# Optimization experiments

Hardware: AMD Instinct MI355X
Metric: run time of the kernel (lower is better)

The kernel has to match this reference:

```python
import jax, jax.numpy as jnp
import numpy as np

V, E, D_ENC, H, A, NF, K = 96, 64, 256, 256, 128, 10, 5
B, T_ENC, T_TGT = 64, 1024, 256


def setup_inputs() -> dict:
    key = jax.random.key(0)
    ks = jax.random.split(key, 16)
    s = 0.05
    emb = jax.random.normal(ks[0], (V, E), jnp.float32) * s
    emb = emb.at[0].set(0.0)  # padding_idx=0
    inp = {
        "encoder_outputs": jax.random.normal(ks[1], (B, T_ENC, D_ENC), jnp.float32),
        "encoder_lengths": jax.random.randint(ks[2], (B,), 1, T_ENC + 1),
        "targets": jax.random.randint(ks[3], (B, T_TGT), 0, V),
        "emb": emb,
        "W_ih": jax.random.normal(ks[4], (4 * H, E + D_ENC), jnp.float32) * s,
        "W_hh": jax.random.normal(ks[5], (4 * H, H), jnp.float32) * s,
        "b_ih": jax.random.normal(ks[6], (4 * H,), jnp.float32) * s,
        "b_hh": jax.random.normal(ks[7], (4 * H,), jnp.float32) * s,
        "conv_w": jax.random.normal(ks[8], (NF, 1, K), jnp.float32) * s,
        "W_enc": jax.random.normal(ks[9], (A, D_ENC), jnp.float32) * s,
        "W_dec": jax.random.normal(ks[10], (A, H), jnp.float32) * s,
        "W_loc": jax.random.normal(ks[11], (A, NF), jnp.float32) * s,
        "v_w": jax.random.normal(ks[12], (1, A), jnp.float32) * s,
        "out_w1": jax.random.normal(ks[13], (H, H + D_ENC), jnp.float32) * s,
        "out_b1": jax.random.normal(ks[14], (H,), jnp.float32) * s,
        "out_w2": jax.random.normal(ks[15], (V, H), jnp.float32) * s,
        "out_b2": jnp.zeros((V,), jnp.float32),
    }
    return inp


def _forward(encoder_outputs, encoder_lengths, targets, emb, W_ih, W_hh, b_ih,
             b_hh, conv_w, W_enc, W_dec, W_loc, v_w, out_w1, out_b1, out_w2, out_b2):
    dtype = encoder_outputs.dtype
    b, t_enc, d_enc = encoder_outputs.shape
    mask = jnp.arange(t_enc)[None, :] < encoder_lengths[:, None]  # [B, T_enc]
    enc_proj = encoder_outputs @ W_enc.T  # [B, T_enc, A] (weights fixed -> hoisted)
    bias = b_ih + b_hh
    pad = (K - 1) // 2

    tok_emb = emb[targets[:, :-1]]          # [B, T_dec, E]
    tok_emb = jnp.swapaxes(tok_emb, 0, 1)   # [T_dec, B, E] for scan

    h0 = jnp.zeros((b, H), dtype)
    c0 = jnp.zeros((b, H), dtype)
    ctx0 = jnp.zeros((b, d_enc), dtype)
    aw0 = jnp.full((b, t_enc), 1.0 / t_enc, dtype)

    def step(carry, e_t):
        h, c, ctx, aw = carry
        # LSTM cell (PyTorch gate order i, f, g, o)
        x = jnp.concatenate([e_t, ctx], axis=-1)            # [B, E+D_enc]
        gates = x @ W_ih.T + h @ W_hh.T + bias              # [B, 4H]
        i, f, g, o = jnp.split(gates, 4, axis=-1)
        c = jax.nn.sigmoid(f) * c + jax.nn.sigmoid(i) * jnp.tanh(g)
        h = jax.nn.sigmoid(o) * jnp.tanh(c)
        # location-sensitive attention
        loc = jax.lax.conv_general_dilated(aw[:, None, :], conv_w, (1,),
                                           [(pad, pad)],
                                           dimension_numbers=("NCH", "OIH", "NCH"))
        loc = jnp.swapaxes(loc, 1, 2)                       # [B, T_enc, NF]
        energy_in = enc_proj + (h @ W_dec.T)[:, None, :] + loc @ W_loc.T
        energy = jnp.tanh(energy_in) @ v_w[0]               # [B, T_enc]
        energy = jnp.where(mask, energy, -1e9)
        aw = jax.nn.softmax(energy, axis=1)
        ctx = jnp.einsum("bt,btd->bd", aw, encoder_outputs)
        # output MLP (dropout = identity at eval)
        hid = jnp.tanh(jnp.concatenate([h, ctx], axis=-1) @ out_w1.T + out_b1)
        logits = hid @ out_w2.T + out_b2                    # [B, V]
        return (h, c, ctx, aw), logits

    _, logits = jax.lax.scan(step, (h0, c0, ctx0, aw0), tok_emb)
    return jnp.swapaxes(logits, 0, 1)  # [B, T_dec, V]


def reference(encoder_outputs, encoder_lengths, targets, emb, W_ih, W_hh, b_ih,
              b_hh, conv_w, W_enc, W_dec, W_loc, v_w, out_w1, out_b1, out_w2, out_b2):
    return _forward(encoder_outputs, encoder_lengths, targets, emb, W_ih, W_hh,
                    b_ih, b_hh, conv_w, W_enc, W_dec, W_loc, v_w, out_w1,
                    out_b1, out_w2, out_b2)
```

## Files before the change

### kernel.cpp

```cpp
#include <hip/hip_runtime.h>
#include <hip/hip_bf16.h>

#define BB   64
#define TENC 1024
#define DENC 256
#define HN   256
#define AN   128
#define NFC  10
#define EMBD 64
#define VN   96
#define TT   255

typedef unsigned short u16;

__device__ __forceinline__ float fsig(float x){ return 1.0f/(1.0f+__expf(-x)); }
__device__ __forceinline__ float ftanh(float x){ return 1.0f - 2.0f/(1.0f+__expf(2.0f*x)); }
__device__ __forceinline__ float b2f(u16 v){ return __uint_as_float(((unsigned)v) << 16); }
__device__ __forceinline__ u16 f2b(float x){
    __hip_bfloat16 h = __float2bfloat16(x);
    return *reinterpret_cast<u16*>(&h);
}
__device__ __forceinline__ float4 ld_bf4(const u16* p){
    ushort4 v = *(const ushort4*)p;
    return make_float4(b2f(v.x), b2f(v.y), b2f(v.z), b2f(v.w));
}

struct Params {
    const u16* encb; const u16* enc_projb; const u16* WdecTb;
    const float* conv_w; const float* W_loc; const float* v_w;
    const int* lengths; const int* targets; const float* emb;
    const float* WcombP; const float* biasw;
    const float* W1T; const float* out_b1; const float* W2T; const float* out_b2;
    float* e0; float* e1; float* ctxU0; float* ctxU1; float* SU0; float* SU1;
    float* h0; float* h1; float* c_st; float* hidA; float* hidB;
    float* out;
};

__global__ void k_prep(const float* __restrict__ enc,
                       const float* __restrict__ W_ih, const float* __restrict__ W_hh,
                       const float* __restrict__ b_ih, const float* __restrict__ b_hh,
                       const float* __restrict__ W_dec, const float* __restrict__ out_w1,
                       const float* __restrict__ out_w2,
                       u16* __restrict__ encb, u16* __restrict__ WdecTb,
                       float* __restrict__ WcombP, float* __restrict__ biasw,
                       float* __restrict__ W1T, float* __restrict__ W2T,
                       float* __restrict__ e_init, float* __restrict__ S_init)
{
    int tid = blockIdx.x*blockDim.x + threadIdx.x;
    int tot = blockDim.x*gridDim.x;
    for (size_t i = tid; i < (size_t)BB*TENC*DENC; i += tot) encb[i] = f2b(enc[i]);
    for (int i = tid; i < 576*1024; i += tot){
        int k = i >> 10, rp = i & 1023;
        int ug = rp >> 4, q = rp & 15, gidx = q >> 2, ul = q & 3;
        int g = gidx*256 + ug*4 + ul;
        WcombP[i] = (k < 320) ? W_ih[(size_t)g*320 + k] : W_hh[(size_t)g*256 + (k-320)];
    }
    for (int i = tid; i < 1024; i += tot) biasw[i] = b_ih[i] + b_hh[i];
    for (int i = tid; i < 256*128; i += tot){ int u = i>>7, a = i&127; WdecTb[i] = f2b(W_dec[a*256 + u]); }
    for (int i = tid; i < 512*256; i += tot){ int k = i>>8, r = i&255; W1T[i] = out_w1[(size_t)r*512 + k]; }
    for (int i = tid; i < 256*96;  i += tot){ int k = i/96, v = i - k*96; W2T[i] = out_w2[(size_t)v*256 + k]; }
    for (int i = tid; i < BB*TENC; i += tot) e_init[i] = 1.0f;
    for (int i = tid; i < BB; i += tot) S_init[i] = (float)TENC;
}

__global__ __launch_bounds__(128) void k_encproj(const float* __restrict__ enc,
                                                 const float* __restrict__ W_enc,
                                                 u16* __restrict__ enc_projb)
{
    __shared__ float rows[32][256];
    int r0 = blockIdx.x * 32;
    for (int i = threadIdx.x; i < 32*256; i += 128)
        rows[i>>8][i&255] = enc[(size_t)r0*256 + i];
    __syncthreads();
    int a = threadIdx.x;
    float acc[32];
    #pragma unroll
    for (int r=0;r<32;r++) acc[r]=0.f;
    const float* w = W_enc + a*256;
    for (int d=0; d<256; d+=4){
        float4 wv = *(const float4*)(w + d);
        #pragma unroll
        for (int r=0;r<32;r++){
            float4 rv = *(const float4*)(&rows[r][d]);
            acc[r] += wv.x*rv.x + wv.y*rv.y + wv.z*rv.z + wv.w*rv.w;
        }
    }
    for (int r=0;r<32;r++) enc_projb[(size_t)(r0+r)*AN + a] = f2b(acc[r]);
}

union alignas(16) SMemCell {
    struct { float xh[8][584]; float part[4][16][9]; float gates[8][17]; } gat;
};
union alignas(16) SMemAtt {
    struct { float hdec[128]; float part[256]; float ehalo[68]; float cw[52];
             float loc[64][11]; float wlocT[10*128]; float evals[64];
             float ep[64][33]; float wacc[4][256]; } att;
    struct { float xh[8][520]; float part[4][16][9]; } hidm;
    struct { float hs[8][260]; float part[4][32][9]; } lgt;
};

__global__ __launch_bounds__(256) void k_cell(Params P, int t)
{
    __shared__ SMemCell u;
    const int blk = blockIdx.x, tid = threadIdx.x;
    const int wr = t & 1;
    const float* ctxU_r = wr ? P.ctxU0 : P.ctxU1;
    float*       ctxU_w = wr ? P.ctxU1 : P.ctxU0;
    const float* SU_r   = wr ? P.SU0   : P.SU1;
    float*       SU_w   = wr ? P.SU1   : P.SU0;
    const float* h_old  = wr ? P.h0    : P.h1;
    float*       h_new  = wr ? P.h1    : P.h0;

    const int ug = blk & 63, bg = blk >> 6;
    const int b0 = bg*8;
    if (ug == 1){
        for (int i = tid; i < 8*DENC; i += 256) ctxU_w[b0*DENC + i] = 0.f;
        if (tid < 8) SU_w[b0 + tid] = 0.f;
    }
    for (int i = tid; i < 8*EMBD; i += 256){
        int bl = i>>6, j = i&63;
        int tok = P.targets[(b0+bl)*256 + t];
        u.gat.xh[bl][j] = P.emb[tok*EMBD + j];
    }
    for (int i = tid; i < 8*HN; i += 256){
        int bl = i>>8, d = i&255;
        u.gat.xh[bl][320+d] = (t == 0) ? 0.f : h_old[(b0+bl)*HN + d];
    }
    for (int i = tid; i < 8*DENC; i += 256){
        int bl = i>>8, d = i&255;
        u.gat.xh[bl][64+d] = (t == 0) ? 0.f
            : ctxU_r[(b0+bl)*DENC + d] * (1.0f/SU_r[b0+bl]);
    }
    __syncthreads();
    {
        const int kq = tid >> 6, lane = tid & 63, rl = lane & 15, blq = lane >> 4;
        const int rowP = ug*16 + rl, bl0 = blq*2;
        const float* wp  = P.WcombP + (size_t)(kq*144)*1024 + rowP;
        const float* x0p = &u.gat.xh[bl0][kq*144];
        const float* x1p = &u.gat.xh[bl0+1][kq*144];
        float s0 = 0.f, s1 = 0.f;
        for (int k = 0; k < 144; k += 4){
            float w0 = wp[0], w1 = wp[1024], w2 = wp[2048], w3 = wp[3072]; wp += 4096;
            float4 xa = *(const float4*)(x0p + k);
            float4 xb = *(const float4*)(x1p + k);
            s0 += w0*xa.x + w1*xa.y + w2*xa.z + w3*xa.w;
            s1 += w0*xb.x + w1*xb.y + w2*xb.z + w3*xb.w;
        }
        u.gat.part[kq][rl][bl0] = s0; u.gat.part[kq][rl][bl0+1] = s1;
    }
    __syncthreads();
    if (tid < 128){
        int bl = tid >> 4, rl = tid & 15;
        float s = u.gat.part[0][rl][bl] + u.gat.part[1][rl][bl]
                + u.gat.part[2][rl][bl] + u.gat.part[3][rl][bl];
        int gidx = rl >> 2, ul = rl & 3;
        u.gat.gates[bl][rl] = s + P.biasw[gidx*256 + ug*4 + ul];
    }
    __syncthreads();
    if (tid < 32){
        int bl = tid >> 2, ul = tid & 3;
        int bgl = b0 + bl, unit = ug*4 + ul;
        float gi = u.gat.gates[bl][0+ul],  gf = u.gat.gates[bl][4+ul];
        float gg = u.gat.gates[bl][8+ul],  go = u.gat.gates[bl][12+ul];
        float cold = (t == 0) ? 0.f : P.c_st[bgl*HN + unit];
        float cn = fsig(gf)*cold + fsig(gi)*ftanh(gg);
        P.c_st[bgl*HN + unit] = cn;
        h_new[bgl*HN + unit] = fsig(go)*ftanh(cn);
    }
}

__global__ __launch_bounds__(256) void k_att(Params P, int t)
{
    __shared__ SMemAtt u;
    const int blk = blockIdx.x, tid = threadIdx.x;
    const int wr = t & 1;
    const float* ctxU_r = wr ? P.ctxU0 : P.ctxU1;
    float*       ctxU_w = wr ? P.ctxU1 : P.ctxU0;
    const float* SU_r   = wr ? P.SU0   : P.SU1;
    float*       SU_w   = wr ? P.SU1   : P.SU0;
    const float* h_old  = wr ? P.h0    : P.h1;
    const float* h_new  = wr ? P.h1    : P.h0;
    const float* hid_pv = wr ? P.hidA  : P.hidB;
    float*       hid_nw = wr ? P.hidB  : P.hidA;
    const float* e_prev = wr ? P.e0    : P.e1;
    float*       e_new  = wr ? P.e1    : P.e0;

    if (blk < 512){
        if (t > 254) return;
        const int b = blk >> 3;
        const int q = blk & 7;
        const int len = P.lengths[b];
        const float invS = 1.0f / SU_r[b];

        if (tid < 50) u.att.cw[tid] = P.conv_w[tid];
        for (int i = tid; i < 1280; i += 256){
            int f = i >> 7, a = i & 127;
            u.att.wlocT[f*128 + a] = P.W_loc[a*NFC + f];
        }
        {
            int a = tid & 127, half = tid >> 7;
            const u16* wd = P.WdecTb + (size_t)(half*128)*AN + a;
            const float* hb = h_new + b*HN + half*128;
            float s0 = 0.f, s1 = 0.f;
            #pragma unroll 4
            for (int uu = 0; uu < 128; uu += 2){
                s0 += hb[uu]   * b2f(wd[(size_t)uu*AN]);
                s1 += hb[uu+1] * b2f(wd[(size_t)(uu+1)*AN]);
            }
            u.att.part[tid] = s0 + s1;
        }
        __syncthreads();
        if (tid < 128) u.att.hdec[tid] = u.att.part[tid] + u.att.part[tid+128];
        __syncthreads();

        for (int kk = 0; kk < 2; kk++){
            const int ch = q + 8*kk;
            const int t0 = ch*64;
            float* e_row = e_new + b*TENC + t0;
            int nv = len - t0; nv = nv < 0 ? 0 : (nv > 64 ? 64 : nv);
            if (nv == 0){
                if (tid < 64) e_row[tid] = 0.f;
                continue;
            }
            __syncthreads();
            if (tid < 68){
                int g = t0 - 2 + tid;
                u.att.ehalo[tid] = (g >= 0 && g < TENC) ? e_prev[b*TENC + g] : 0.f;
            }
            __syncthreads();
            if (tid < 64){
                #pragma unroll
                for (int f = 0; f < NFC; f++){
                    float s = 0.f;
                    #pragma unroll
                    for (int k2 = 0; k2 < 5; k2++) s += u.att.ehalo[tid+k2] * u.att.cw[f*5+k2];
                    u.att.loc[tid][f] = s * invS;
                }
            }
            __syncthreads();

            {
                const int ag = tid & 31, pg = tid >> 5;
                const int a0 = ag*4;
                float4 hd4 = *(const float4*)&u.att.hdec[a0];
                float4 vv  = *(const float4*)(P.v_w + a0);
                const u16* epr = P.enc_projb + ((size_t)(b*TENC + t0))*AN + a0;
                #pragma unroll
                for (int i = 0; i < 8; i++){
                    int p = pg*8 + i;
                    if (p < nv){
                        float4 er = ld_bf4(epr + (size_t)p*AN);
                        float x0 = er.x + hd4.x, x1 = er.y + hd4.y;
                        float x2 = er.z + hd4.z, x3 = er.w + hd4.w;
                        #pragma unroll
                        for (int f = 0; f < NFC; f++){
                            float lf = u.att.loc[p][f];
                            const float* wla = &u.att.wlocT[f*128 + a0];
                            x0 += lf*wla[0]; x1 += lf*wla[1]; x2 += lf*wla[2]; x3 += lf*wla[3];
                        }
                        u.att.ep[p][ag] = vv.x*ftanh(x0) + vv.y*ftanh(x1)
                                        + vv.z*ftanh(x2) + vv.w*ftanh(x3);
                    }
                }
            }
            __syncthreads();

            if (tid < 64){
                int p = tid;
                float e = 0.f;
                if (p < nv){
                    float s0 = 0.f, s1 = 0.f;
                    #pragma unroll
                    for (int j = 0; j < 32; j += 2){ s0 += u.att.ep[p][j]; s1 += u.att.ep[p][j+1]; }
                    e = __expf(s0 + s1);
                }
                u.att.evals[p] = e;
                e_row[p] = e;
                float se = e;
                #pragma unroll
                for (int off = 32; off; off >>= 1) se += __shfl_xor(se, off);
                if (tid == 0) atomicAdd(SU_w + b, se);
            }
            __syncthreads();

            {
                const int dq = tid & 63, pq = tid >> 6;
                const u16* encb = P.encb + ((size_t)(b*TENC + t0))*DENC + dq*4;
                float ax=0.f, ay=0.f, az=0.f, aw=0.f;
                for (int i = 0; i < 16; i++){
                    int p = pq + i*4;
                    if (p < nv){
                        float ev = u.att.evals[p];
                        float4 ex = ld_bf4(encb + (size_t)p*DENC);
                        ax += ev*ex.x; ay += ev*ex.y; az += ev*ex.z; aw += ev*ex.w;
                    }
                }
                float4 r; r.x=ax; r.y=ay; r.z=az; r.w=aw;
                *(float4*)&u.att.wacc[pq][dq*4] = r;
            }
            __syncthreads();
            {
                int d = tid;
                float s = u.att.wacc[0][d] + u.att.wacc[1][d]
                        + u.att.wacc[2][d] + u.att.wacc[3][d];
                atomicAdd(ctxU_w + b*DENC + d, s);
            }
            __syncthreads();
        }
        return;
    }

    if (blk < 640){
        if (!(t >= 1 && t <= 255)) return;
        int hb = blk - 512;
        int bg = hb >> 4, rg = hb & 15;
        int b0 = bg*8, r0 = rg*16;
        for (int i = tid; i < 8*HN; i += 256){
            int bl = i>>8, d = i&255;
            u.hidm.xh[bl][d] = h_old[(b0+bl)*HN + d];
        }
        for (int i = tid; i < 8*DENC; i += 256){
            int bl = i>>8, d = i&255;
            u.hidm.xh[bl][256+d] = ctxU_r[(b0+bl)*DENC + d] * (1.0f/SU_r[b0+bl]);
        }
        __syncthreads();
        {
            const int kq = tid >> 6, lane = tid & 63, rl = lane & 15, blq = lane >> 4;
            const int bl0 = blq*2;
            const float* wp  = P.W1T + (size_t)(kq*128)*256 + (r0 + rl);
            const float* x0p = &u.hidm.xh[bl0][kq*128];
            const float* x1p = &u.hidm.xh[bl0+1][kq*128];
            float s0 = 0.f, s1 = 0.f;
            for (int k = 0; k < 128; k += 4){
                float w0 = wp[0], w1 = wp[256], w2 = wp[512], w3 = wp[768]; wp += 1024;
                float4 xa = *(const float4*)(x0p + k);
                float4 xb = *(const float4*)(x1p + k);
                s0 += w0*xa.x + w1*xa.y + w2*xa.z + w3*xa.w;
                s1 += w0*xb.x + w1*xb.y + w2*xb.z + w3*xb.w;
            }
            u.hidm.part[kq][rl][bl0] = s0; u.hidm.part[kq][rl][bl0+1] = s1;
        }
        __syncthreads();
        if (tid < 128){
            int bl = tid >> 4, rl = tid & 15;
            int r = r0 + rl;
            float s = u.hidm.part[0][rl][bl] + u.hidm.part[1][rl][bl]
                    + u.hidm.part[2][rl][bl] + u.hidm.part[3][rl][bl];
            hid_nw[(b0+bl)*HN + r] = ftanh(s + P.out_b1[r]);
        }
        return;
    }

    {
        if (t < 2) return;
        int lt = blk - 640;
        int bgr = lt/3, vg = lt%3;
        int b0 = bgr*8, v0 = vg*32;
        for (int i = tid; i < 8*HN; i += 256){
            int bl = i>>8, d = i&255;
            u.lgt.hs[bl][d] = hid_pv[(b0+bl)*HN + d];
        }
        __syncthreads();
        {
            const int kq = tid >> 6, lane = tid & 63, vl = lane & 31, blq = lane >> 5;
            const int bl0 = blq*4;
            const float* wp = P.W2T + (size_t)(kq*64)*96 + (v0 + vl);
            float a4[4] = {0.f,0.f,0.f,0.f};
            for (int k = 0; k < 64; k += 4){
                float w0 = wp[0], w1 = wp[96], w2 = wp[192], w3 = wp[288]; wp += 384;
                #pragma unroll
                for (int j = 0; j < 4; j++){
                    float4 x = *(const float4*)&u.lgt.hs[bl0+j][kq*64 + k];
                    a4[j] += w0*x.x + w1*x.y + w2*x.z + w3*x.w;
                }
            }
            #pragma unroll
            for (int j = 0; j < 4; j++) u.lgt.part[kq][vl][bl0+j] = a4[j];
        }
        __syncthreads();
        {
            int bl = tid >> 5, vl = tid & 31;
            int v = v0 + vl;
            float s = u.lgt.part[0][vl][bl] + u.lgt.part[1][vl][bl]
                    + u.lgt.part[2][vl][bl] + u.lgt.part[3][vl][bl];
            P.out[((size_t)(b0+bl)*TT + (t-2))*VN + v] = s + P.out_b2[v];
        }
    }
}

extern "C" void kernel_launch(void* const* d_in, const int* in_sizes, int n_in,
                              void* d_out, int out_size, void* d_ws, size_t ws_size,
                              hipStream_t stream)
{
    const float* enc     = (const float*)d_in[0];
    const int*   lengths = (const int*)  d_in[1];
    const int*   targets = (const int*)  d_in[2];
    const float* emb     = (const float*)d_in[3];
    const float* W_ih    = (const float*)d_in[4];
    const float* W_hh    = (const float*)d_in[5];
    const float* b_ih    = (const float*)d_in[6];
    const float* b_hh    = (const float*)d_in[7];
    const float* conv_w  = (const float*)d_in[8];
    const float* W_enc   = (const float*)d_in[9];
    const float* W_dec   = (const float*)d_in[10];
    const float* W_loc   = (const float*)d_in[11];
    const float* v_w     = (const float*)d_in[12];
    const float* out_w1  = (const float*)d_in[13];
    const float* out_b1  = (const float*)d_in[14];
    const float* out_w2  = (const float*)d_in[15];
    const float* out_b2  = (const float*)d_in[16];
    float* out = (float*)d_out;

    float* ws = (float*)d_ws;
    size_t off = 0;
    auto alloc = [&](size_t n){ float* p = ws + off; off += n; return p; };
    u16*   encb      = (u16*)  alloc((size_t)BB*TENC*DENC/2);
    u16*   enc_projb = (u16*)  alloc((size_t)BB*TENC*AN/2);
    u16*   WdecTb    = (u16*)  alloc(256*128/2);
    float* WcombP    = alloc(576*1024);
    float* biasw     = alloc(1024);
    float* W1T       = alloc(512*256);
    float* W2T       = alloc(256*96);
    float* e0        = alloc(BB*TENC);
    float* e1        = alloc(BB*TENC);
    float* ctxU0     = alloc(BB*DENC);
    float* ctxU1     = alloc(BB*DENC);
    float* SU0       = alloc(BB);
    float* SU1       = alloc(BB);
    float* h0        = alloc(BB*HN);
    float* h1        = alloc(BB*HN);
    float* c_st      = alloc(BB*HN);
    float* hidA      = alloc(BB*HN);
    float* hidB      = alloc(BB*HN);
    if (off * sizeof(float) > ws_size) return;

    k_prep<<<dim3(512), dim3(256), 0, stream>>>(enc, W_ih, W_hh, b_ih, b_hh, W_dec,
                                                out_w1, out_w2,
                                                encb, WdecTb, WcombP, biasw, W1T, W2T,
                                                e1, SU1);
    k_encproj<<<dim3(2048), dim3(128), 0, stream>>>(enc, W_enc, enc_projb);

    Params pr;
    pr.encb = encb; pr.enc_projb = enc_projb; pr.WdecTb = WdecTb;
    pr.conv_w = conv_w; pr.W_loc = W_loc; pr.v_w = v_w;
    pr.lengths = lengths; pr.targets = targets; pr.emb = emb;
    pr.WcombP = WcombP; pr.biasw = biasw;
    pr.W1T = W1T; pr.out_b1 = out_b1; pr.W2T = W2T; pr.out_b2 = out_b2;
    pr.e0 = e0; pr.e1 = e1; pr.ctxU0 = ctxU0; pr.ctxU1 = ctxU1;
    pr.SU0 = SU0; pr.SU1 = SU1; pr.h0 = h0; pr.h1 = h1;
    pr.c_st = c_st; pr.hidA = hidA; pr.hidB = hidB; pr.out = out;

    for (int t = 0; t <= 256; t++){
        if (t <= 254)
            k_cell<<<dim3(512), dim3(256), 0, stream>>>(pr, t);
        k_att<<<dim3(664), dim3(256), 0, stream>>>(pr, t);
    }
}
```

Before: 12.09 ms.

## Rebalance per-step kernels: move conv and output MLP into cell kernel, split attention finer

Each timestep is reorganised. The cell kernel now also runs, in 64 extra blocks, the location convolution (written to a bf16 buffer), the output hidden layer and the logits, one batch row per block. The attention kernel becomes 1024 blocks, one per (batch, 64-position chunk), with W_loc held in registers and the convolution results read from global memory. The goal is to spread attention work across more blocks, remove the per-chunk conv sync chain and shorten the critical path. In exchange it adds a global round-trip for the conv features and rounds them to bf16, and the per-row MLP blocks do scalar matvecs with less weight reuse.

After: 12.37 ms. 2.3% more time.

```diff
diff --git a/kernel.cpp b/kernel.cpp
--- a/kernel.cpp
+++ b/kernel.cpp
@@ -33,21 +33,21 @@
     const float* W1T; const float* out_b1; const float* W2T; const float* out_b2;
     float* e0; float* e1; float* ctxU0; float* ctxU1; float* SU0; float* SU1;
     float* h0; float* h1; float* c_st; float* hidA; float* hidB;
+    u16* locb;
     float* out;
 };
 
-__global__ void k_prep(const float* __restrict__ enc,
+__global__ void k_prep(Params P, const float* __restrict__ enc,
                        const float* __restrict__ W_ih, const float* __restrict__ W_hh,
                        const float* __restrict__ b_ih, const float* __restrict__ b_hh,
                        const float* __restrict__ W_dec, const float* __restrict__ out_w1,
-                       const float* __restrict__ out_w2,
-                       u16* __restrict__ encb, u16* __restrict__ WdecTb,
-                       float* __restrict__ WcombP, float* __restrict__ biasw,
-                       float* __restrict__ W1T, float* __restrict__ W2T,
-                       float* __restrict__ e_init, float* __restrict__ S_init)
+                       const float* __restrict__ out_w2)
 {
     int tid = blockIdx.x*blockDim.x + threadIdx.x;
     int tot = blockDim.x*gridDim.x;
+    u16* encb = (u16*)P.encb;  u16* WdecTb = (u16*)P.WdecTb;
+    float* WcombP = (float*)P.WcombP; float* biasw = (float*)P.biasw;
+    float* W1T = (float*)P.W1T; float* W2T = (float*)P.W2T;
     for (size_t i = tid; i < (size_t)BB*TENC*DENC; i += tot) encb[i] = f2b(enc[i]);
     for (int i = tid; i < 576*1024; i += tot){
         int k = i >> 10, rp = i & 1023;
@@ -59,8 +59,8 @@
     for (int i = tid; i < 256*128; i += tot){ int u = i>>7, a = i&127; WdecTb[i] = f2b(W_dec[a*256 + u]); }
     for (int i = tid; i < 512*256; i += tot){ int k = i>>8, r = i&255; W1T[i] = out_w1[(size_t)r*512 + k]; }
     for (int i = tid; i < 256*96;  i += tot){ int k = i/96, v = i - k*96; W2T[i] = out_w2[(size_t)v*256 + k]; }
-    for (int i = tid; i < BB*TENC; i += tot) e_init[i] = 1.0f;
-    for (int i = tid; i < BB; i += tot) S_init[i] = (float)TENC;
+    for (int i = tid; i < BB*TENC; i += tot) P.e1[i] = 1.0f;
+    for (int i = tid; i < BB; i += tot) P.SU1[i] = (float)TENC;
 }
 
 __global__ __launch_bounds__(128) void k_encproj(const float* __restrict__ enc,
@@ -88,20 +88,18 @@
     for (int r=0;r<32;r++) enc_projb[(size_t)(r0+r)*AN + a] = f2b(acc[r]);
 }
 
-union alignas(16) SMemCell {
+union alignas(16) SMemU {
     struct { float xh[8][584]; float part[4][16][9]; float gates[8][17]; } gat;
-};
-union alignas(16) SMemAtt {
-    struct { float hdec[128]; float part[256]; float ehalo[68]; float cw[52];
-             float loc[64][11]; float wlocT[10*128]; float evals[64];
+    struct { float hbuf[256]; float part[256]; float loc[64][11]; float evals[64];
              float ep[64][33]; float wacc[4][256]; } att;
-    struct { float xh[8][520]; float part[4][16][9]; } hidm;
-    struct { float hs[8][260]; float part[4][32][9]; } lgt;
+    struct { float erow[1036]; float cw[52]; } convt;
+    struct { float xh[512]; } hid2;
+    struct { float hs[256]; } lg2;
 };
 
 __global__ __launch_bounds__(256) void k_cell(Params P, int t)
 {
-    __shared__ SMemCell u;
+    __shared__ SMemU u;
     const int blk = blockIdx.x, tid = threadIdx.x;
     const int wr = t & 1;
     const float* ctxU_r = wr ? P.ctxU0 : P.ctxU1;
@@ -110,281 +108,239 @@
     float*       SU_w   = wr ? P.SU1   : P.SU0;
     const float* h_old  = wr ? P.h0    : P.h1;
     float*       h_new  = wr ? P.h1    : P.h0;
-
-    const int ug = blk & 63, bg = blk >> 6;
-    const int b0 = bg*8;
-    if (ug == 1){
-        for (int i = tid; i < 8*DENC; i += 256) ctxU_w[b0*DENC + i] = 0.f;
-        if (tid < 8) SU_w[b0 + tid] = 0.f;
-    }
-    for (int i = tid; i < 8*EMBD; i += 256){
-        int bl = i>>6, j = i&63;
-        int tok = P.targets[(b0+bl)*256 + t];
-        u.gat.xh[bl][j] = P.emb[tok*EMBD + j];
-    }
-    for (int i = tid; i < 8*HN; i += 256){
-        int bl = i>>8, d = i&255;
-        u.gat.xh[bl][320+d] = (t == 0) ? 0.f : h_old[(b0+bl)*HN + d];
-    }
-    for (int i = tid; i < 8*DENC; i += 256){
-        int bl = i>>8, d = i&255;
-        u.gat.xh[bl][64+d] = (t == 0) ? 0.f
-            : ctxU_r[(b0+bl)*DENC + d] * (1.0f/SU_r[b0+bl]);
-    }
-    __syncthreads();
-    {
-        const int kq = tid >> 6, lane = tid & 63, rl = lane & 15, blq = lane >> 4;
-        const int rowP = ug*16 + rl, bl0 = blq*2;
-        const float* wp  = P.WcombP + (size_t)(kq*144)*1024 + rowP;
-        const float* x0p = &u.gat.xh[bl0][kq*144];
-        const float* x1p = &u.gat.xh[bl0+1][kq*144];
-        float s0 = 0.f, s1 = 0.f;
-        for (int k = 0; k < 144; k += 4){
-            float w0 = wp[0], w1 = wp[1024], w2 = wp[2048], w3 = wp[3072]; wp += 4096;
-            float4 xa = *(const float4*)(x0p + k);
-            float4 xb = *(const float4*)(x1p + k);
-            s0 += w0*xa.x + w1*xa.y + w2*xa.z + w3*xa.w;
-            s1 += w0*xb.x + w1*xb.y + w2*xb.z + w3*xb.w;
-        }
-        u.gat.part[kq][rl][bl0] = s0; u.gat.part[kq][rl][bl0+1] = s1;
-    }
-    __syncthreads();
-    if (tid < 128){
-        int bl = tid >> 4, rl = tid & 15;
-        float s = u.gat.part[0][rl][bl] + u.gat.part[1][rl][bl]
-                + u.gat.part[2][rl][bl] + u.gat.part[3][rl][bl];
-        int gidx = rl >> 2, ul = rl & 3;
-        u.gat.gates[bl][rl] = s + P.biasw[gidx*256 + ug*4 + ul];
-    }
-    __syncthreads();
-    if (tid < 32){
-        int bl = tid >> 2, ul = tid & 3;
-        int bgl = b0 + bl, unit = ug*4 + ul;
-        float gi = u.gat.gates[bl][0+ul],  gf = u.gat.gates[bl][4+ul];
-        float gg = u.gat.gates[bl][8+ul],  go = u.gat.gates[bl][12+ul];
-        float cold = (t == 0) ? 0.f : P.c_st[bgl*HN + unit];
-        float cn = fsig(gf)*cold + fsig(gi)*ftanh(gg);
-        P.c_st[bgl*HN + unit] = cn;
-        h_new[bgl*HN + unit] = fsig(go)*ftanh(cn);
-    }
-}
-
-__global__ __launch_bounds__(256) void k_att(Params P, int t)
-{
-    __shared__ SMemAtt u;
-    const int blk = blockIdx.x, tid = threadIdx.x;
-    const int wr = t & 1;
-    const float* ctxU_r = wr ? P.ctxU0 : P.ctxU1;
-    float*       ctxU_w = wr ? P.ctxU1 : P.ctxU0;
-    const float* SU_r   = wr ? P.SU0   : P.SU1;
-    float*       SU_w   = wr ? P.SU1   : P.SU0;
-    const float* h_old  = wr ? P.h0    : P.h1;
-    const float* h_new  = wr ? P.h1    : P.h0;
     const float* hid_pv = wr ? P.hidA  : P.hidB;
     float*       hid_nw = wr ? P.hidB  : P.hidA;
     const float* e_prev = wr ? P.e0    : P.e1;
-    float*       e_new  = wr ? P.e1    : P.e0;
 
     if (blk < 512){
         if (t > 254) return;
-        const int b = blk >> 3;
-        const int q = blk & 7;
-        const int len = P.lengths[b];
-        const float invS = 1.0f / SU_r[b];
-
-        if (tid < 50) u.att.cw[tid] = P.conv_w[tid];
-        for (int i = tid; i < 1280; i += 256){
-            int f = i >> 7, a = i & 127;
-            u.att.wlocT[f*128 + a] = P.W_loc[a*NFC + f];
-        }
-        {
-            int a = tid & 127, half = tid >> 7;
-            const u16* wd = P.WdecTb + (size_t)(half*128)*AN + a;
-            const float* hb = h_new + b*HN + half*128;
-            float s0 = 0.f, s1 = 0.f;
-            #pragma unroll 4
-            for (int uu = 0; uu < 128; uu += 2){
-                s0 += hb[uu]   * b2f(wd[(size_t)uu*AN]);
-                s1 += hb[uu+1] * b2f(wd[(size_t)(uu+1)*AN]);
-            }
-            u.att.part[tid] = s0 + s1;
-        }
-        __syncthreads();
-        if (tid < 128) u.att.hdec[tid] = u.att.part[tid] + u.att.part[tid+128];
-        __syncthreads();
-
-        for (int kk = 0; kk < 2; kk++){
-            const int ch = q + 8*kk;
-            const int t0 = ch*64;
-            float* e_row = e_new + b*TENC + t0;
-            int nv = len - t0; nv = nv < 0 ? 0 : (nv > 64 ? 64 : nv);
-            if (nv == 0){
-                if (tid < 64) e_row[tid] = 0.f;
-                continue;
-            }
-            __syncthreads();
-            if (tid < 68){
-                int g = t0 - 2 + tid;
-                u.att.ehalo[tid] = (g >= 0 && g < TENC) ? e_prev[b*TENC + g] : 0.f;
-            }
-            __syncthreads();
-            if (tid < 64){
-                #pragma unroll
-                for (int f = 0; f < NFC; f++){
-                    float s = 0.f;
-                    #pragma unroll
-                    for (int k2 = 0; k2 < 5; k2++) s += u.att.ehalo[tid+k2] * u.att.cw[f*5+k2];
-                    u.att.loc[tid][f] = s * invS;
-                }
-            }
-            __syncthreads();
-
-            {
-                const int ag = tid & 31, pg = tid >> 5;
-                const int a0 = ag*4;
-                float4 hd4 = *(const float4*)&u.att.hdec[a0];
-                float4 vv  = *(const float4*)(P.v_w + a0);
-                const u16* epr = P.enc_projb + ((size_t)(b*TENC + t0))*AN + a0;
-                #pragma unroll
-                for (int i = 0; i < 8; i++){
-                    int p = pg*8 + i;
-                    if (p < nv){
-                        float4 er = ld_bf4(epr + (size_t)p*AN);
-                        float x0 = er.x + hd4.x, x1 = er.y + hd4.y;
-                        float x2 = er.z + hd4.z, x3 = er.w + hd4.w;
-                        #pragma unroll
-                        for (int f = 0; f < NFC; f++){
-                            float lf = u.att.loc[p][f];
-                            const float* wla = &u.att.wlocT[f*128 + a0];
-                            x0 += lf*wla[0]; x1 += lf*wla[1]; x2 += lf*wla[2]; x3 += lf*wla[3];
-                        }
-                        u.att.ep[p][ag] = vv.x*ftanh(x0) + vv.y*ftanh(x1)
-                                        + vv.z*ftanh(x2) + vv.w*ftanh(x3);
-                    }
-                }
-            }
-            __syncthreads();
-
-            if (tid < 64){
-                int p = tid;
-                float e = 0.f;
-                if (p < nv){
-                    float s0 = 0.f, s1 = 0.f;
-                    #pragma unroll
-                    for (int j = 0; j < 32; j += 2){ s0 += u.att.ep[p][j]; s1 += u.att.ep[p][j+1]; }
-                    e = __expf(s0 + s1);
-                }
-                u.att.evals[p] = e;
-                e_row[p] = e;
-                float se = e;
-                #pragma unroll
-                for (int off = 32; off; off >>= 1) se += __shfl_xor(se, off);
-                if (tid == 0) atomicAdd(SU_w + b, se);
-            }
-            __syncthreads();
-
-            {
-                const int dq = tid & 63, pq = tid >> 6;
-                const u16* encb = P.encb + ((size_t)(b*TENC + t0))*DENC + dq*4;
-                float ax=0.f, ay=0.f, az=0.f, aw=0.f;
-                for (int i = 0; i < 16; i++){
-                    int p = pq + i*4;
-                    if (p < nv){
-                        float ev = u.att.evals[p];
-                        float4 ex = ld_bf4(encb + (size_t)p*DENC);
-                        ax += ev*ex.x; ay += ev*ex.y; az += ev*ex.z; aw += ev*ex.w;
-                    }
-                }
-                float4 r; r.x=ax; r.y=ay; r.z=az; r.w=aw;
-                *(float4*)&u.att.wacc[pq][dq*4] = r;
-            }
-            __syncthreads();
-            {
-                int d = tid;
-                float s = u.att.wacc[0][d] + u.att.wacc[1][d]
-                        + u.att.wacc[2][d] + u.att.wacc[3][d];
-                atomicAdd(ctxU_w + b*DENC + d, s);
-            }
-            __syncthreads();
-        }
-        return;
-    }
-
-    if (blk < 640){
-        if (!(t >= 1 && t <= 255)) return;
-        int hb = blk - 512;
-        int bg = hb >> 4, rg = hb & 15;
-        int b0 = bg*8, r0 = rg*16;
+        const int ug = blk & 63, bg = blk >> 6;
+        const int b0 = bg*8;
+        if (ug == 1){
+            for (int i = tid; i < 8*DENC; i += 256) ctxU_w[b0*DENC + i] = 0.f;
+            if (tid < 8) SU_w[b0 + tid] = 0.f;
+        }
+        for (int i = tid; i < 8*EMBD; i += 256){
+            int bl = i>>6, jj = i&63;
+            int tok = P.targets[(b0+bl)*256 + t];
+            u.gat.xh[bl][jj] = P.emb[tok*EMBD + jj];
+        }
         for (int i = tid; i < 8*HN; i += 256){
             int bl = i>>8, d = i&255;
-            u.hidm.xh[bl][d] = h_old[(b0+bl)*HN + d];
+            u.gat.xh[bl][320+d] = (t == 0) ? 0.f : h_old[(b0+bl)*HN + d];
         }
         for (int i = tid; i < 8*DENC; i += 256){
             int bl = i>>8, d = i&255;
-            u.hidm.xh[bl][256+d] = ctxU_r[(b0+bl)*DENC + d] * (1.0f/SU_r[b0+bl]);
+            u.gat.xh[bl][64+d] = (t == 0) ? 0.f
+                : ctxU_r[(b0+bl)*DENC + d] * (1.0f/SU_r[b0+bl]);
         }
         __syncthreads();
         {
             const int kq = tid >> 6, lane = tid & 63, rl = lane & 15, blq = lane >> 4;
-            const int bl0 = blq*2;
-            const float* wp  = P.W1T + (size_t)(kq*128)*256 + (r0 + rl);
-            const float* x0p = &u.hidm.xh[bl0][kq*128];
-            const float* x1p = &u.hidm.xh[bl0+1][kq*128];
+            const int rowP = ug*16 + rl, bl0 = blq*2;
+            const float* wp  = P.WcombP + (size_t)(kq*144)*1024 + rowP;
+            const float* x0p = &u.gat.xh[bl0][kq*144];
+            const float* x1p = &u.gat.xh[bl0+1][kq*144];
             float s0 = 0.f, s1 = 0.f;
-            for (int k = 0; k < 128; k += 4){
-                float w0 = wp[0], w1 = wp[256], w2 = wp[512], w3 = wp[768]; wp += 1024;
+            for (int k = 0; k < 144; k += 4){
+                float w0 = wp[0], w1 = wp[1024], w2 = wp[2048], w3 = wp[3072]; wp += 4096;
                 float4 xa = *(const float4*)(x0p + k);
                 float4 xb = *(const float4*)(x1p + k);
                 s0 += w0*xa.x + w1*xa.y + w2*xa.z + w3*xa.w;
                 s1 += w0*xb.x + w1*xb.y + w2*xb.z + w3*xb.w;
             }
-            u.hidm.part[kq][rl][bl0] = s0; u.hidm.part[kq][rl][bl0+1] = s1;
+            u.gat.part[kq][rl][bl0] = s0; u.gat.part[kq][rl][bl0+1] = s1;
         }
         __syncthreads();
         if (tid < 128){
             int bl = tid >> 4, rl = tid & 15;
-            int r = r0 + rl;
-            float s = u.hidm.part[0][rl][bl] + u.hidm.part[1][rl][bl]
-                    + u.hidm.part[2][rl][bl] + u.hidm.part[3][rl][bl];
-            hid_nw[(b0+bl)*HN + r] = ftanh(s + P.out_b1[r]);
+            float s = u.gat.part[0][rl][bl] + u.gat.part[1][rl][bl]
+                    + u.gat.part[2][rl][bl] + u.gat.part[3][rl][bl];
+            int gidx = rl >> 2, ul = rl & 3;
+            u.gat.gates[bl][rl] = s + P.biasw[gidx*256 + ug*4 + ul];
+        }
+        __syncthreads();
+        if (tid < 32){
+            int bl = tid >> 2, ul = tid & 3;
+            int bgl = b0 + bl, unit = ug*4 + ul;
+            float gi = u.gat.gates[bl][0+ul],  gf = u.gat.gates[bl][4+ul];
+            float gg = u.gat.gates[bl][8+ul],  go = u.gat.gates[bl][12+ul];
+            float cold = (t == 0) ? 0.f : P.c_st[bgl*HN + unit];
+            float cn = fsig(gf)*cold + fsig(gi)*ftanh(gg);
+            P.c_st[bgl*HN + unit] = cn;
+            h_new[bgl*HN + unit] = fsig(go)*ftanh(cn);
         }
         return;
     }
 
+    const int bb = blk - 512;
+    if (t <= 254){
+        const float invS = 1.0f / SU_r[bb];
+        for (int i = tid; i < 1028; i += 256){
+            int g = i - 2;
+            u.convt.erow[i] = (g >= 0 && g < TENC) ? e_prev[bb*TENC + g] : 0.f;
+        }
+        if (tid < 50) u.convt.cw[tid] = P.conv_w[tid];
+        __syncthreads();
+        for (int it = 0; it < 4; it++){
+            int p = tid + it*256;
+            u16* lp = P.locb + (size_t)(bb*TENC + p)*NFC;
+            #pragma unroll
+            for (int f = 0; f < NFC; f++){
+                float s = 0.f;
+                #pragma unroll
+                for (int k2 = 0; k2 < 5; k2++) s += u.convt.erow[p+k2] * u.convt.cw[f*5+k2];
+                lp[f] = f2b(s * invS);
+            }
+        }
+    }
+    if (t >= 1 && t <= 255){
+        __syncthreads();
+        const float invS = 1.0f / SU_r[bb];
+        u.hid2.xh[tid]       = h_old[bb*HN + tid];
+        u.hid2.xh[256 + tid] = ctxU_r[bb*DENC + tid] * invS;
+        __syncthreads();
+        const float* wp = P.W1T + tid;
+        float a0=0.f, a1=0.f, a2=0.f, a3=0.f;
+        for (int k = 0; k < 512; k += 4){
+            a0 += wp[(size_t)(k+0)*256] * u.hid2.xh[k+0];
+            a1 += wp[(size_t)(k+1)*256] * u.hid2.xh[k+1];
+            a2 += wp[(size_t)(k+2)*256] * u.hid2.xh[k+2];
+            a3 += wp[(size_t)(k+3)*256] * u.hid2.xh[k+3];
+        }
+        hid_nw[bb*HN + tid] = ftanh((a0+a1)+(a2+a3) + P.out_b1[tid]);
+    }
+    if (t >= 2){
+        __syncthreads();
+        u.lg2.hs[tid] = hid_pv[bb*HN + tid];
+        __syncthreads();
+        if (tid < VN){
+            const float* wp = P.W2T + tid;
+            float a0=0.f, a1=0.f, a2=0.f, a3=0.f;
+            for (int k = 0; k < 256; k += 4){
+                a0 += wp[(size_t)(k+0)*96] * u.lg2.hs[k+0];
+                a1 += wp[(size_t)(k+1)*96] * u.lg2.hs[k+1];
+                a2 += wp[(size_t)(k+2)*96] * u.lg2.hs[k+2];
+                a3 += wp[(size_t)(k+3)*96] * u.lg2.hs[k+3];
+            }
+            P.out[((size_t)bb*TT + (t-2))*VN + tid] = (a0+a1)+(a2+a3) + P.out_b2[tid];
+        }
+    }
+}
+
+__global__ __launch_bounds__(256) void k_att(Params P, int t)
+{
+    __shared__ SMemU u;
+    const int blk = blockIdx.x, tid = threadIdx.x;
+    const int wr = t & 1;
+    float*       ctxU_w = wr ? P.ctxU1 : P.ctxU0;
+    float*       SU_w   = wr ? P.SU1   : P.SU0;
+    const float* h_new  = wr ? P.h1    : P.h0;
+    float*       e_new  = wr ? P.e1    : P.e0;
+
+    const int b  = blk & 63;
+    const int ch = blk >> 6;
+    const int t0 = ch*64;
+    float* e_row = e_new + b*TENC + t0;
+    const int len = P.lengths[b];
+    int nv = len - t0; nv = nv < 0 ? 0 : (nv > 64 ? 64 : nv);
+    if (nv == 0){
+        if (tid < 64) e_row[tid] = 0.f;
+        return;
+    }
+
+    const int ag = tid & 31, pg = tid >> 5;
+    const int a0 = ag*4;
+    float4 vv = *(const float4*)(P.v_w + a0);
+    float4 wl[NFC];
+    #pragma unroll
+    for (int f = 0; f < NFC; f++){
+        wl[f].x = P.W_loc[(a0+0)*NFC+f]; wl[f].y = P.W_loc[(a0+1)*NFC+f];
+        wl[f].z = P.W_loc[(a0+2)*NFC+f]; wl[f].w = P.W_loc[(a0+3)*NFC+f];
+    }
+    u.att.hbuf[tid] = h_new[b*HN + tid];
     {
-        if (t < 2) return;
-        int lt = blk - 640;
-        int bgr = lt/3, vg = lt%3;
-        int b0 = bgr*8, v0 = vg*32;
-        for (int i = tid; i < 8*HN; i += 256){
-            int bl = i>>8, d = i&255;
-            u.lgt.hs[bl][d] = hid_pv[(b0+bl)*HN + d];
-        }
-        __syncthreads();
-        {
-            const int kq = tid >> 6, lane = tid & 63, vl = lane & 31, blq = lane >> 5;
-            const int bl0 = blq*4;
-            const float* wp = P.W2T + (size_t)(kq*64)*96 + (v0 + vl);
-            float a4[4] = {0.f,0.f,0.f,0.f};
-            for (int k = 0; k < 64; k += 4){
-                float w0 = wp[0], w1 = wp[96], w2 = wp[192], w3 = wp[288]; wp += 384;
+        const u16* lsrc = P.locb + (size_t)(b*TENC + t0)*NFC;
+        for (int i = tid; i < 640; i += 256)
+            u.att.loc[i/10][i%10] = b2f(lsrc[i]);
+    }
+    __syncthreads();
+    {
+        int a = tid & 127, half = tid >> 7;
+        const u16* wd = P.WdecTb + (size_t)(half*128)*AN + a;
+        const float* hb = &u.att.hbuf[half*128];
+        float s0 = 0.f, s1 = 0.f;
+        #pragma unroll 4
+        for (int uu = 0; uu < 128; uu += 2){
+            s0 += hb[uu]   * b2f(wd[(size_t)uu*AN]);
+            s1 += hb[uu+1] * b2f(wd[(size_t)(uu+1)*AN]);
+        }
+        u.att.part[tid] = s0 + s1;
+    }
+    __syncthreads();
+    {
+        float4 hd4;
+        hd4.x = u.att.part[a0+0] + u.att.part[128+a0+0];
+        hd4.y = u.att.part[a0+1] + u.att.part[128+a0+1];
+        hd4.z = u.att.part[a0+2] + u.att.part[128+a0+2];
+        hd4.w = u.att.part[a0+3] + u.att.part[128+a0+3];
+        const u16* epr = P.enc_projb + ((size_t)(b*TENC + t0))*AN + a0;
+        #pragma unroll
+        for (int i = 0; i < 8; i++){
+            int p = pg*8 + i;
+            if (p < nv){
+                float4 er = ld_bf4(epr + (size_t)p*AN);
+                float x0 = er.x + hd4.x, x1 = er.y + hd4.y;
+                float x2 = er.z + hd4.z, x3 = er.w + hd4.w;
                 #pragma unroll
-                for (int j = 0; j < 4; j++){
-                    float4 x = *(const float4*)&u.lgt.hs[bl0+j][kq*64 + k];
-                    a4[j] += w0*x.x + w1*x.y + w2*x.z + w3*x.w;
+                for (int f = 0; f < NFC; f++){
+                    float lf = u.att.loc[p][f];
+                    x0 += lf*wl[f].x; x1 += lf*wl[f].y;
+                    x2 += lf*wl[f].z; x3 += lf*wl[f].w;
                 }
+                u.att.ep[p][ag] = vv.x*ftanh(x0) + vv.y*ftanh(x1)
+                                + vv.z*ftanh(x2) + vv.w*ftanh(x3);
             }
+        }
+    }
+    __syncthreads();
+    if (tid < 64){
+        int p = tid;
+        float e = 0.f;
+        if (p < nv){
+            float s0 = 0.f, s1 = 0.f;
             #pragma unroll
-            for (int j = 0; j < 4; j++) u.lgt.part[kq][vl][bl0+j] = a4[j];
-        }
-        __syncthreads();
-        {
-            int bl = tid >> 5, vl = tid & 31;
-            int v = v0 + vl;
-            float s = u.lgt.part[0][vl][bl] + u.lgt.part[1][vl][bl]
-                    + u.lgt.part[2][vl][bl] + u.lgt.part[3][vl][bl];
-            P.out[((size_t)(b0+bl)*TT + (t-2))*VN + v] = s + P.out_b2[v];
-        }
+            for (int j2 = 0; j2 < 32; j2 += 2){ s0 += u.att.ep[p][j2]; s1 += u.att.ep[p][j2+1]; }
+            e = __expf(s0 + s1);
+        }
+        u.att.evals[p] = e;
+        e_row[p] = e;
+        float se = e;
+        #pragma unroll
+        for (int off = 32; off; off >>= 1) se += __shfl_xor(se, off);
+        if (tid == 0) atomicAdd(SU_w + b, se);
+    }
+    __syncthreads();
+    {
+        const int dq = tid & 63, pq = tid >> 6;
+        const u16* encb = P.encb + ((size_t)(b*TENC + t0))*DENC + dq*4;
+        float ax=0.f, ay=0.f, az=0.f, aw=0.f;
+        for (int i = 0; i < 16; i++){
+            int p = pq + i*4;
+            if (p < nv){
+                float ev = u.att.evals[p];
+                float4 ex = ld_bf4(encb + (size_t)p*DENC);
+                ax += ev*ex.x; ay += ev*ex.y; az += ev*ex.z; aw += ev*ex.w;
+            }
+        }
+        float4 r; r.x=ax; r.y=ay; r.z=az; r.w=aw;
+        *(float4*)&u.att.wacc[pq][dq*4] = r;
+    }
+    __syncthreads();
+    {
+        float s = u.att.wacc[0][tid] + u.att.wacc[1][tid]
+                + u.att.wacc[2][tid] + u.att.wacc[3][tid];
+        atomicAdd(ctxU_w + b*DENC + tid, s);
     }
 }
 
@@ -432,13 +388,8 @@
     float* c_st      = alloc(BB*HN);
     float* hidA      = alloc(BB*HN);
     float* hidB      = alloc(BB*HN);
+    u16*   locb      = (u16*)  alloc((size_t)BB*TENC*NFC/2);
     if (off * sizeof(float) > ws_size) return;
-
-    k_prep<<<dim3(512), dim3(256), 0, stream>>>(enc, W_ih, W_hh, b_ih, b_hh, W_dec,
-                                                out_w1, out_w2,
-                                                encb, WdecTb, WcombP, biasw, W1T, W2T,
-                                                e1, SU1);
-    k_encproj<<<dim3(2048), dim3(128), 0, stream>>>(enc, W_enc, enc_projb);
 
     Params pr;
     pr.encb = encb; pr.enc_projb = enc_projb; pr.WdecTb = WdecTb;
@@ -448,11 +399,16 @@
     pr.W1T = W1T; pr.out_b1 = out_b1; pr.W2T = W2T; pr.out_b2 = out_b2;
     pr.e0 = e0; pr.e1 = e1; pr.ctxU0 = ctxU0; pr.ctxU1 = ctxU1;
     pr.SU0 = SU0; pr.SU1 = SU1; pr.h0 = h0; pr.h1 = h1;
-    pr.c_st = c_st; pr.hidA = hidA; pr.hidB = hidB; pr.out = out;
+    pr.c_st = c_st; pr.hidA = hidA; pr.hidB = hidB;
+    pr.locb = locb; pr.out = out;
+
+    k_prep<<<dim3(512), dim3(256), 0, stream>>>(pr, enc, W_ih, W_hh, b_ih, b_hh, W_dec,
+                                                out_w1, out_w2);
+    k_encproj<<<dim3(2048), dim3(128), 0, stream>>>(enc, W_enc, enc_projb);
 
     for (int t = 0; t <= 256; t++){
+        k_cell<<<dim3(576), dim3(256), 0, stream>>>(pr, t);
         if (t <= 254)
-            k_cell<<<dim3(512), dim3(256), 0, stream>>>(pr, t);
-        k_att<<<dim3(664), dim3(256), 0, stream>>>(pr, t);
-    }
-}
+            k_att<<<dim3(1024), dim3(256), 0, stream>>>(pr, t);
+    }
+}
```
